# Kernel tuning notes

Hardware: AMD Instinct MI355X
Metric: run time of the kernel (lower is better)

The kernel has to match this reference:

```python
import jax, jax.numpy as jnp
import numpy as np

HEADS = 12
HEAD_DIM = 64          # dim_out // heads = 768 // 12
Q_STRIDE = 4
WINDOW_SIZE = 16       # post-pool tokens per window; pre-pool = Q_STRIDE*WINDOW_SIZE = 64
DIM = 768
DIM_OUT = 768


def setup_inputs() -> dict:
    key = jax.random.key(0)
    k1, k2, k3 = jax.random.split(key, 3)
    B, N = 32, 3136
    x = jax.random.normal(k1, (B, N, DIM), dtype=jnp.float32)
    Wqkv = jax.random.normal(k2, (DIM, 3 * DIM_OUT), dtype=jnp.float32) * 0.02
    bqkv = jnp.zeros((3 * DIM_OUT,), dtype=jnp.float32)
    Wproj = jax.random.normal(k3, (DIM_OUT, DIM_OUT), dtype=jnp.float32) * 0.02
    bproj = jnp.zeros((DIM_OUT,), dtype=jnp.float32)
    return {"x": x, "Wqkv": Wqkv, "bqkv": bqkv, "Wproj": Wproj, "bproj": bproj}


def reference(x, Wqkv, bqkv, Wproj, bproj):
    B, N, _ = x.shape
    num_windows = N // (Q_STRIDE * WINDOW_SIZE)  # 49
    scale = HEAD_DIM ** (-0.5)

    # QKV projection (torch Linear uses x @ W^T; here Wqkv is stored [dim, 3*dim_out])
    qkv = x @ Wqkv + bqkv                                  # [B, N, 3*dim_out]
    # Same reshape as torch: windows are the inner split of the token axis
    qkv = qkv.reshape(B, N // num_windows, num_windows, 3, HEADS, HEAD_DIM)
    qkv = jnp.transpose(qkv, (3, 0, 4, 2, 1, 5))           # [3, B, h, w, t, d]
    q, k, v = qkv[0], qkv[1], qkv[2]                       # t = Q_STRIDE*WINDOW_SIZE

    # Query max-pooling over stride groups
    q = q.reshape(B, HEADS, num_windows, Q_STRIDE, WINDOW_SIZE, HEAD_DIM).max(axis=3)
    # q: [B, h, w, WINDOW_SIZE, d]

    # Scaled dot-product attention within each window
    logits = jnp.einsum('bhwqd,bhwkd->bhwqk', q, k) * scale
    attn = jax.nn.softmax(logits, axis=-1)
    o = jnp.einsum('bhwqk,bhwkd->bhwqd', attn, v)          # [B, h, w, q, d]

    # transpose(1,3) then flatten tokens, channels = heads*head_dim
    o = jnp.transpose(o, (0, 3, 2, 1, 4)).reshape(B, -1, DIM_OUT)
    return o @ Wproj + bproj
```

## Files before the change

### kernel.cpp

```cpp
#include <hip/hip_runtime.h>
#include <hip/hip_bf16.h>


typedef __bf16 bf16x8 __attribute__((ext_vector_type(8)));
typedef float f32x4 __attribute__((ext_vector_type(4)));
typedef unsigned short u16x8 __attribute__((ext_vector_type(8)));

#define GLOBAL_AS __attribute__((address_space(1)))
#define LDS_AS __attribute__((address_space(3)))

__device__ __forceinline__ unsigned short f2bf(float f) {
    unsigned u = __builtin_bit_cast(unsigned, f);
    u += 0x7FFFu + ((u >> 16) & 1u);
    return (unsigned short)(u >> 16);
}
__device__ __forceinline__ float bf2f(unsigned short h) {
    return __builtin_bit_cast(float, (unsigned)h << 16);
}

__device__ __forceinline__ void load16_to_lds(const void* g, void* l) {
    __builtin_amdgcn_global_load_lds((const GLOBAL_AS unsigned int*)g,
                                     (LDS_AS unsigned int*)l, 16, 0, 0);
}

__global__ void cvt_f32_bf16(const float* __restrict__ in,
                             unsigned short* __restrict__ out, long n4) {
    long i = (long)blockIdx.x * blockDim.x + threadIdx.x;
    if (i >= n4) return;
    float4 f = ((const float4*)in)[i];
    uint2 u;
    u.x = (unsigned)f2bf(f.x) | ((unsigned)f2bf(f.y) << 16);
    u.y = (unsigned)f2bf(f.z) | ((unsigned)f2bf(f.w) << 16);
    ((uint2*)out)[i] = u;
}

__global__ void transpose_cvt(const float* __restrict__ W,
                              unsigned short* __restrict__ Wt, int K, int N) {
    __shared__ float tile[32][33];
    int bx = blockIdx.x * 32;
    int by = blockIdx.y * 32;
    int tx = threadIdx.x & 31, ty = threadIdx.x >> 5;
    #pragma unroll
    for (int i = 0; i < 32; i += 8)
        tile[ty + i][tx] = W[(size_t)(by + ty + i) * N + bx + tx];
    __syncthreads();
    #pragma unroll
    for (int i = 0; i < 32; i += 8)
        Wt[(size_t)(bx + ty + i) * K + by + tx] = f2bf(tile[tx][ty + i]);
}

#define VM_WAIT4 asm volatile("s_waitcnt vmcnt(4)" ::: "memory")
#define VM_WAIT0 asm volatile("s_waitcnt vmcnt(0)" ::: "memory")

#define GPHASE(BUF, KSR, IH, LOADBG, STG, WAITS) do {                        \
    if (LOADBG) {                                                            \
        const unsigned short* bb =                                           \
            &ls[(BUF) * 32768 + 16384 + (KSR) * 8192 + colOff];              \
        bg[0] = *(const bf16x8*)&bb[(wn +  0 + lane15) * 32];                \
        bg[1] = *(const bf16x8*)&bb[(wn + 16 + lane15) * 32];                \
        bg[2] = *(const bf16x8*)&bb[(wn + 32 + lane15) * 32];                \
        bg[3] = *(const bf16x8*)&bb[(wn + 48 + lane15) * 32];                \
    }                                                                        \
    {                                                                        \
        const unsigned short* ab =                                           \
            &ls[(BUF) * 32768 + (KSR) * 8192 + colOff];                      \
        af[0] = *(const bf16x8*)&ab[(wm + (IH)*64 +  0 + lane15) * 32];      \
        af[1] = *(const bf16x8*)&ab[(wm + (IH)*64 + 16 + lane15) * 32];      \
        af[2] = *(const bf16x8*)&ab[(wm + (IH)*64 + 32 + lane15) * 32];      \
        af[3] = *(const bf16x8*)&ab[(wm + (IH)*64 + 48 + lane15) * 32];      \
    }                                                                        \
    STG;                                                                     \
    WAITS;                                                                   \
    __builtin_amdgcn_s_barrier();                                            \
    asm volatile("s_waitcnt lgkmcnt(0)" ::: "memory");                       \
    __builtin_amdgcn_sched_barrier(0);                                       \
    __builtin_amdgcn_s_setprio(1);                                           \
    _Pragma("unroll")                                                        \
    for (int ii = 0; ii < 4; ++ii)                                           \
        _Pragma("unroll")                                                    \
        for (int j = 0; j < 4; ++j)                                          \
            acc[(IH)*4 + ii][j] = __builtin_amdgcn_mfma_f32_16x16x32_bf16(   \
                bg[j], af[ii], acc[(IH)*4 + ii][j], 0, 0, 0);                \
    __builtin_amdgcn_s_setprio(0);                                           \
    __builtin_amdgcn_s_barrier();                                            \
} while (0)

template <bool OUT_BF16>
__global__ __launch_bounds__(512, 2)
void gemm_bt256(const unsigned short* __restrict__ A,
                const unsigned short* __restrict__ Bt,
                const float* __restrict__ bias,
                void* __restrict__ Cv, int M, int N, int K) {
    __shared__ alignas(16) unsigned short ls[65536];

    const int tid  = threadIdx.x;
    const int lane = tid & 63;
    const int wave = tid >> 6;
    const int wm = (wave >> 2) * 128;
    const int wn = (wave & 3) * 64;
    const int lane15 = lane & 15;
    const int quad   = lane >> 4;
    const int colOff = ((quad ^ (lane15 & 3)) * 8);

    const int nwg = (int)(gridDim.x * gridDim.y);
    const int hid = (int)(blockIdx.y * gridDim.x + blockIdx.x);
    const int q8  = nwg >> 3, r8 = nwg & 7;
    const int xcd = hid & 7;
    const int lid = (xcd < r8 ? xcd * (q8 + 1) : r8 * (q8 + 1) + (xcd - r8) * q8)
                    + (hid >> 3);
    const int tileX = lid % (int)gridDim.x;
    const int tileY = lid / (int)gridDim.x;
    const long bm = (long)tileY * 256;
    const long bn = (long)tileX * 256;

    const int r0 = tid >> 2;
    const int lc = (tid & 3) ^ (r0 & 3);
    const unsigned short* gA0 = A  + (bm + r0)       * (long)K + lc * 8;
    const unsigned short* gA1 = A  + (bm + r0 + 128) * (long)K + lc * 8;
    const unsigned short* gB0 = Bt + (bn + r0)       * (long)K + lc * 8;
    const unsigned short* gB1 = Bt + (bn + r0 + 128) * (long)K + lc * 8;
    const int ldsWaveBase = wave * 512;

    auto STAGE = [&](int buf, int op, int ksr, int kt) {
        const int ko = kt * 64 + ksr * 32;
        unsigned short* d = &ls[buf * 32768 + op * 16384 + ksr * 8192 + ldsWaveBase];
        if (op == 0) {
            load16_to_lds(gA0 + ko, d);
            load16_to_lds(gA1 + ko, d + 4096);
        } else {
            load16_to_lds(gB0 + ko, d);
            load16_to_lds(gB1 + ko, d + 4096);
        }
    };

    f32x4 acc[8][4] = {};
    bf16x8 af[4], bg[4];

    const int NT = K >> 6;
    const int NI = NT >> 1;

    STAGE(0, 0, 0, 0); STAGE(0, 1, 0, 0); STAGE(0, 0, 1, 0); STAGE(0, 1, 1, 0);
    STAGE(1, 0, 0, 1); STAGE(1, 1, 0, 1);
    VM_WAIT4;
    __builtin_amdgcn_s_barrier();

    for (int i = 0; i < NI; ++i) {
        const int t2 = 2 * i;
        const bool last = (i == NI - 1);
        GPHASE(0, 0, 0, 1, { STAGE(1, 0, 1, t2 + 1); }, { (void)0; });
        GPHASE(0, 0, 1, 0, { STAGE(1, 1, 1, t2 + 1); }, { (void)0; });
        GPHASE(0, 1, 0, 1, { if (!last) STAGE(0, 0, 0, t2 + 2); }, { (void)0; });
        GPHASE(0, 1, 1, 0, { if (!last) STAGE(0, 1, 0, t2 + 2); },
               { if (last) { VM_WAIT0; } else { VM_WAIT4; } });
        GPHASE(1, 0, 0, 1, { if (!last) STAGE(0, 0, 1, t2 + 2); }, { (void)0; });
        GPHASE(1, 0, 1, 0, { if (!last) STAGE(0, 1, 1, t2 + 2); }, { (void)0; });
        GPHASE(1, 1, 0, 1, { if (!last) STAGE(1, 0, 0, t2 + 3); }, { (void)0; });
        GPHASE(1, 1, 1, 0, { if (!last) { STAGE(1, 1, 0, t2 + 3); VM_WAIT4; } },
               { (void)0; });
    }

    const long rbase = bm + wm + lane15;
    const int  cbase = (int)bn + wn + quad * 4;
    #pragma unroll
    for (int j = 0; j < 4; ++j) {
        const int col = cbase + j * 16;
        const float4 bv = *(const float4*)&bias[col];
        #pragma unroll
        for (int i = 0; i < 8; ++i) {
            const long row = rbase + i * 16;
            const size_t idx = (size_t)row * N + col;
            const float v0 = acc[i][j][0] + bv.x;
            const float v1 = acc[i][j][1] + bv.y;
            const float v2 = acc[i][j][2] + bv.z;
            const float v3 = acc[i][j][3] + bv.w;
            if constexpr (OUT_BF16) {
                ushort4 s;
                s.x = f2bf(v0); s.y = f2bf(v1); s.z = f2bf(v2); s.w = f2bf(v3);
                *(ushort4*)((unsigned short*)Cv + idx) = s;
            } else {
                float4 s;
                s.x = v0; s.y = v1; s.z = v2; s.w = v3;
                *(float4*)((float*)Cv + idx) = s;
            }
        }
    }
}

__global__ __launch_bounds__(256)
void attn_win_mfma(const unsigned short* __restrict__ qkv,
                   unsigned short* __restrict__ o) {
    const int hg = blockIdx.x;
    const int w  = blockIdx.y;
    const int b  = blockIdx.z;
    const int wave = threadIdx.x >> 6;
    const int lane = threadIdx.x & 63;
    const int h = hg * 4 + wave;
    const int l = lane & 15;
    const int quad = lane >> 4;

    __shared__ alignas(16) unsigned short vT[4][64 * 72];
    __shared__ alignas(16) unsigned short ps[4][16 * 72];

    const long tokStride = 49L * 2304;
    const long base = ((long)b * 3136 + w) * 2304 + h * 64;

    bf16x8 af[2];
    {
        const unsigned short* qr = qkv + base + (long)l * tokStride + quad * 8;
        float m0[8], m1[8];
        #pragma unroll
        for (int sg = 0; sg < 4; ++sg) {
            uint4 u0 = *(const uint4*)(qr + (long)sg * 16 * tokStride);
            uint4 u1 = *(const uint4*)(qr + (long)sg * 16 * tokStride + 32);
            const unsigned short* p0 = (const unsigned short*)&u0;
            const unsigned short* p1 = (const unsigned short*)&u1;
            #pragma unroll
            for (int e = 0; e < 8; ++e) {
                float f0 = bf2f(p0[e]), f1 = bf2f(p1[e]);
                if (sg == 0) { m0[e] = f0; m1[e] = f1; }
                else { m0[e] = fmaxf(m0[e], f0); m1[e] = fmaxf(m1[e], f1); }
            }
        }
        u16x8 a0, a1;
        #pragma unroll
        for (int e = 0; e < 8; ++e) {
            a0[e] = f2bf(m0[e] * 0.125f);
            a1[e] = f2bf(m1[e] * 0.125f);
        }
        af[0] = __builtin_bit_cast(bf16x8, a0);
        af[1] = __builtin_bit_cast(bf16x8, a1);
    }

    {
        const unsigned short* vr = qkv + base + (long)lane * tokStride + 1536;
        unsigned short* vw = &vT[wave][0];
        #pragma unroll
        for (int i = 0; i < 8; ++i) {
            uint4 u = *(const uint4*)(vr + i * 8);
            const unsigned short* pe = (const unsigned short*)&u;
            #pragma unroll
            for (int e = 0; e < 8; ++e)
                vw[(i * 8 + e) * 72 + lane] = pe[e];
        }
    }

    f32x4 Sc[4] = {};
    {
        bf16x8 bk0, bk1;
        #pragma unroll
        for (int tt = 0; tt < 4; ++tt) {
            const unsigned short* kr =
                qkv + base + (long)(tt * 16 + l) * tokStride + 768 + quad * 8;
            bk0 = __builtin_bit_cast(bf16x8, *(const uint4*)kr);
            bk1 = __builtin_bit_cast(bf16x8, *(const uint4*)(kr + 32));
            Sc[tt] = __builtin_amdgcn_mfma_f32_16x16x32_bf16(af[0], bk0, Sc[tt], 0, 0, 0);
            Sc[tt] = __builtin_amdgcn_mfma_f32_16x16x32_bf16(af[1], bk1, Sc[tt], 0, 0, 0);
        }
    }

    float pr[4][4];
    {
        #pragma unroll
        for (int r = 0; r < 4; ++r) {
            float mx = fmaxf(fmaxf(Sc[0][r], Sc[1][r]), fmaxf(Sc[2][r], Sc[3][r]));
            #pragma unroll
            for (int off = 1; off < 16; off <<= 1)
                mx = fmaxf(mx, __shfl_xor(mx, off));
            float sum = 0.f;
            #pragma unroll
            for (int tt = 0; tt < 4; ++tt) {
                pr[tt][r] = __expf(Sc[tt][r] - mx);
                sum += pr[tt][r];
            }
            #pragma unroll
            for (int off = 1; off < 16; off <<= 1)
                sum += __shfl_xor(sum, off);
            const float inv = 1.0f / sum;
            #pragma unroll
            for (int tt = 0; tt < 4; ++tt) pr[tt][r] *= inv;
        }
    }

    {
        unsigned short* pw = &ps[wave][0];
        #pragma unroll
        for (int r = 0; r < 4; ++r)
            #pragma unroll
            for (int tt = 0; tt < 4; ++tt)
                pw[(quad * 4 + r) * 72 + tt * 16 + l] = f2bf(pr[tt][r]);
    }

    f32x4 Oc[4] = {};
    {
        #pragma unroll
        for (int s = 0; s < 2; ++s) {
            bf16x8 ap = *(const bf16x8*)&ps[wave][l * 72 + s * 32 + quad * 8];
            #pragma unroll
            for (int tt = 0; tt < 4; ++tt) {
                bf16x8 bv = *(const bf16x8*)&vT[wave][(tt * 16 + l) * 72 + s * 32 + quad * 8];
                Oc[tt] = __builtin_amdgcn_mfma_f32_16x16x32_bf16(ap, bv, Oc[tt], 0, 0, 0);
            }
        }
    }

    {
        const long obase = ((long)b * 784 + (long)(quad * 4) * 49 + w) * 768 + h * 64 + l;
        #pragma unroll
        for (int tt = 0; tt < 4; ++tt)
            #pragma unroll
            for (int r = 0; r < 4; ++r)
                o[obase + (long)r * 49 * 768 + tt * 16] = f2bf(Oc[tt][r]);
    }
}

extern "C" void kernel_launch(void* const* d_in, const int* in_sizes, int n_in,
                              void* d_out, int out_size, void* d_ws, size_t ws_size,
                              hipStream_t stream) {
    const float* x     = (const float*)d_in[0];
    const float* Wqkv  = (const float*)d_in[1];
    const float* bqkv  = (const float*)d_in[2];
    const float* Wproj = (const float*)d_in[3];
    const float* bproj = (const float*)d_in[4];
    float* out = (float*)d_out;

    const long needed1 = (32L * 3136 * 768 + 32L * 3136 * 2304 +
                          25088L * 768 + 2304L * 768 + 768L * 768) * 2;
    const int C  = (ws_size >= (size_t)needed1) ? 1 : 4;
    const int CB = 32 / C;
    const long XC = (long)CB * 3136 * 768;
    const long QC = (long)CB * 3136 * 2304;

    char* p = (char*)d_ws;
    unsigned short* xb    = (unsigned short*)p; p += XC * 2;
    unsigned short* qkvb  = (unsigned short*)p; p += QC * 2;
    unsigned short* ob    = (unsigned short*)p; p += 25088L * 768 * 2;
    unsigned short* WqkvT = (unsigned short*)p; p += 2304L * 768 * 2;
    unsigned short* WprojT= (unsigned short*)p; p += 768L * 768 * 2;

    transpose_cvt<<<dim3(72, 24), 256, 0, stream>>>(Wqkv, WqkvT, 768, 2304);
    transpose_cvt<<<dim3(24, 24), 256, 0, stream>>>(Wproj, WprojT, 768, 768);

    const int M = CB * 3136;
    for (int c = 0; c < C; ++c) {
        cvt_f32_bf16<<<(int)(XC / 4 / 256), 256, 0, stream>>>(x + (size_t)c * XC, xb, XC / 4);
        gemm_bt256<true><<<dim3(9, M / 256), 512, 0, stream>>>(
            xb, WqkvT, bqkv, qkvb, M, 2304, 768);
        attn_win_mfma<<<dim3(3, 49, CB), 256, 0, stream>>>(
            qkvb, ob + (size_t)c * CB * 784 * 768);
    }
    gemm_bt256<false><<<dim3(3, 98), 512, 0, stream>>>(
        ob, WprojT, bproj, out, 25088, 768, 768);
}
```

Measured before the change: 1.104 ms.

## Use full 64-wide K rows in LDS with 8-way XOR swizzle for GEMM

Changes the LDS tile layout from two 32-column K sub-slabs per operand to a single 64-column row per M/N index, with an 8-chunk XOR swizzle. Global-to-LDS loads now cover 128-byte contiguous row segments per 8 threads, and the staging schedule is redistributed across the eight phases with a vmcnt(2) wait. The intent is more coalesced global loads and fewer bank conflicts. The new load/wait interleaving is delicate, and a wrong vmcnt could race.

```diff
diff --git a/kernel.cpp b/kernel.cpp
--- a/kernel.cpp
+++ b/kernel.cpp
@@ -49,25 +49,23 @@
         Wt[(size_t)(bx + ty + i) * K + by + tx] = f2bf(tile[tx][ty + i]);
 }
 
-#define VM_WAIT4 asm volatile("s_waitcnt vmcnt(4)" ::: "memory")
+#define VM_WAIT2 asm volatile("s_waitcnt vmcnt(2)" ::: "memory")
 #define VM_WAIT0 asm volatile("s_waitcnt vmcnt(0)" ::: "memory")
 
-#define GPHASE(BUF, KSR, IH, LOADBG, STG, WAITS) do {                        \
+#define GPHASE(BUF, CSW, IH, LOADBG, STG, WAITS) do {                        \
     if (LOADBG) {                                                            \
-        const unsigned short* bb =                                           \
-            &ls[(BUF) * 32768 + 16384 + (KSR) * 8192 + colOff];              \
-        bg[0] = *(const bf16x8*)&bb[(wn +  0 + lane15) * 32];                \
-        bg[1] = *(const bf16x8*)&bb[(wn + 16 + lane15) * 32];                \
-        bg[2] = *(const bf16x8*)&bb[(wn + 32 + lane15) * 32];                \
-        bg[3] = *(const bf16x8*)&bb[(wn + 48 + lane15) * 32];                \
+        const unsigned short* bb = &ls[(BUF) * 32768 + 16384 + (CSW)];       \
+        bg[0] = *(const bf16x8*)&bb[(wn +  0 + lane15) * 64];                \
+        bg[1] = *(const bf16x8*)&bb[(wn + 16 + lane15) * 64];                \
+        bg[2] = *(const bf16x8*)&bb[(wn + 32 + lane15) * 64];                \
+        bg[3] = *(const bf16x8*)&bb[(wn + 48 + lane15) * 64];                \
     }                                                                        \
     {                                                                        \
-        const unsigned short* ab =                                           \
-            &ls[(BUF) * 32768 + (KSR) * 8192 + colOff];                      \
-        af[0] = *(const bf16x8*)&ab[(wm + (IH)*64 +  0 + lane15) * 32];      \
-        af[1] = *(const bf16x8*)&ab[(wm + (IH)*64 + 16 + lane15) * 32];      \
-        af[2] = *(const bf16x8*)&ab[(wm + (IH)*64 + 32 + lane15) * 32];      \
-        af[3] = *(const bf16x8*)&ab[(wm + (IH)*64 + 48 + lane15) * 32];      \
+        const unsigned short* ab = &ls[(BUF) * 32768 + (CSW)];               \
+        af[0] = *(const bf16x8*)&ab[(wm + (IH)*64 +  0 + lane15) * 64];      \
+        af[1] = *(const bf16x8*)&ab[(wm + (IH)*64 + 16 + lane15) * 64];      \
+        af[2] = *(const bf16x8*)&ab[(wm + (IH)*64 + 32 + lane15) * 64];      \
+        af[3] = *(const bf16x8*)&ab[(wm + (IH)*64 + 48 + lane15) * 64];      \
     }                                                                        \
     STG;                                                                     \
     WAITS;                                                                   \
@@ -100,7 +98,8 @@
     const int wn = (wave & 3) * 64;
     const int lane15 = lane & 15;
     const int quad   = lane >> 4;
-    const int colOff = ((quad ^ (lane15 & 3)) * 8);
+    const int csw0 = ((quad    ) ^ (lane & 7)) * 8;
+    const int csw1 = ((quad + 4) ^ (lane & 7)) * 8;
 
     const int nwg = (int)(gridDim.x * gridDim.y);
     const int hid = (int)(blockIdx.y * gridDim.x + blockIdx.x);
@@ -113,24 +112,19 @@
     const long bm = (long)tileY * 256;
     const long bn = (long)tileX * 256;
 
-    const int r0 = tid >> 2;
-    const int lc = (tid & 3) ^ (r0 & 3);
-    const unsigned short* gA0 = A  + (bm + r0)       * (long)K + lc * 8;
-    const unsigned short* gA1 = A  + (bm + r0 + 128) * (long)K + lc * 8;
-    const unsigned short* gB0 = Bt + (bn + r0)       * (long)K + lc * 8;
-    const unsigned short* gB1 = Bt + (bn + r0 + 128) * (long)K + lc * 8;
+    const int r0 = tid >> 3;
+    const int lc = (tid & 7) ^ (r0 & 7);
+    const unsigned short* gA = A  + (bm + r0) * (long)K + lc * 8;
+    const unsigned short* gB = Bt + (bn + r0) * (long)K + lc * 8;
     const int ldsWaveBase = wave * 512;
 
-    auto STAGE = [&](int buf, int op, int ksr, int kt) {
-        const int ko = kt * 64 + ksr * 32;
-        unsigned short* d = &ls[buf * 32768 + op * 16384 + ksr * 8192 + ldsWaveBase];
-        if (op == 0) {
-            load16_to_lds(gA0 + ko, d);
-            load16_to_lds(gA1 + ko, d + 4096);
-        } else {
-            load16_to_lds(gB0 + ko, d);
-            load16_to_lds(gB1 + ko, d + 4096);
-        }
+    auto STAGE_A = [&](int buf, int q, int kt) {
+        load16_to_lds(gA + (long)q * 64 * K + kt * 64,
+                      &ls[buf * 32768 + q * 4096 + ldsWaveBase]);
+    };
+    auto STAGE_B = [&](int buf, int q, int kt) {
+        load16_to_lds(gB + (long)q * 64 * K + kt * 64,
+                      &ls[buf * 32768 + 16384 + q * 4096 + ldsWaveBase]);
     };
 
     f32x4 acc[8][4] = {};
@@ -139,23 +133,36 @@
     const int NT = K >> 6;
     const int NI = NT >> 1;
 
-    STAGE(0, 0, 0, 0); STAGE(0, 1, 0, 0); STAGE(0, 0, 1, 0); STAGE(0, 1, 1, 0);
-    STAGE(1, 0, 0, 1); STAGE(1, 1, 0, 1);
-    VM_WAIT4;
+    STAGE_A(0, 0, 0); STAGE_A(0, 1, 0); STAGE_A(0, 2, 0); STAGE_A(0, 3, 0);
+    STAGE_B(0, 0, 0); STAGE_B(0, 1, 0); STAGE_B(0, 2, 0); STAGE_B(0, 3, 0);
+    STAGE_A(1, 0, 1); STAGE_A(1, 2, 1);
+    VM_WAIT2;
     __builtin_amdgcn_s_barrier();
 
     for (int i = 0; i < NI; ++i) {
         const int t2 = 2 * i;
         const bool last = (i == NI - 1);
-        GPHASE(0, 0, 0, 1, { STAGE(1, 0, 1, t2 + 1); }, { (void)0; });
-        GPHASE(0, 0, 1, 0, { STAGE(1, 1, 1, t2 + 1); }, { (void)0; });
-        GPHASE(0, 1, 0, 1, { if (!last) STAGE(0, 0, 0, t2 + 2); }, { (void)0; });
-        GPHASE(0, 1, 1, 0, { if (!last) STAGE(0, 1, 0, t2 + 2); },
-               { if (last) { VM_WAIT0; } else { VM_WAIT4; } });
-        GPHASE(1, 0, 0, 1, { if (!last) STAGE(0, 0, 1, t2 + 2); }, { (void)0; });
-        GPHASE(1, 0, 1, 0, { if (!last) STAGE(0, 1, 1, t2 + 2); }, { (void)0; });
-        GPHASE(1, 1, 0, 1, { if (!last) STAGE(1, 0, 0, t2 + 3); }, { (void)0; });
-        GPHASE(1, 1, 1, 0, { if (!last) { STAGE(1, 1, 0, t2 + 3); VM_WAIT4; } },
+        GPHASE(0, csw0, 0, 1,
+               { STAGE_A(1, 1, t2 + 1); STAGE_A(1, 3, t2 + 1); STAGE_B(1, 0, t2 + 1); },
+               { (void)0; });
+        GPHASE(0, csw0, 1, 0,
+               { STAGE_B(1, 1, t2 + 1); STAGE_B(1, 2, t2 + 1); STAGE_B(1, 3, t2 + 1); },
+               { (void)0; });
+        GPHASE(0, csw1, 0, 1, { (void)0; }, { (void)0; });
+        GPHASE(0, csw1, 1, 0,
+               { if (!last) { STAGE_A(0, 0, t2 + 2); STAGE_A(0, 2, t2 + 2); } },
+               { if (last) { VM_WAIT0; } else { VM_WAIT2; } });
+        GPHASE(1, csw0, 0, 1,
+               { if (!last) { STAGE_A(0, 1, t2 + 2); STAGE_A(0, 3, t2 + 2); } },
+               { (void)0; });
+        GPHASE(1, csw0, 1, 0,
+               { if (!last) { STAGE_B(0, 0, t2 + 2); STAGE_B(0, 1, t2 + 2); } },
+               { (void)0; });
+        GPHASE(1, csw1, 0, 1,
+               { if (!last) { STAGE_B(0, 2, t2 + 2); STAGE_B(0, 3, t2 + 2); } },
+               { (void)0; });
+        GPHASE(1, csw1, 1, 0,
+               { if (!last) { STAGE_A(1, 0, t2 + 3); STAGE_A(1, 2, t2 + 3); VM_WAIT2; } },
                { (void)0; });
     }
 
```

Result: no change. 1.091 ms (-1.2%).
